# Kernel tuning notes

Measured on AMD Instinct MI355X. Metric: run time of the kernel, lower is better.

Reference implementation:

```python
import jax, jax.numpy as jnp
import numpy as np

N_X = 65536
N_IND = 1024
N_DESC = 64
INIT_LS = 10.0  # initial_lengthscale; params store -log(ls)


def setup_inputs() -> dict:
    key = jax.random.key(0)
    k1, k2, k3, k4 = jax.random.split(key, 4)
    x = jax.random.normal(k1, (N_X, N_DESC), dtype=jnp.float32)
    inducing_x = jax.random.normal(k2, (N_IND, N_DESC), dtype=jnp.float32)
    alpha = jax.random.normal(k3, (N_IND,), dtype=jnp.float32)
    # ARD lengthscales param, initialized near -log(initial_lengthscale) with jitter
    lengthscales = (-np.log(INIT_LS)
                    + 0.1 * jax.random.normal(k4, (N_DESC,), dtype=jnp.float32))
    return {"x": x, "inducing_x": inducing_x, "alpha": alpha,
            "lengthscales": lengthscales.astype(jnp.float32)}


def reference(x, inducing_x, alpha, lengthscales):
    # Squared distance weighted by per-descriptor lengthscale:
    #   d[i, j] = sum_k (x[j,k] - z[i,k])^2 / exp(ls[k])
    # Expanded as ||xw||^2 + ||zw||^2 - 2 zw @ xw^T to avoid the
    # (n_ind, n_x, n_desc) broadcast intermediate (same math).
    inv_sqrt_ls = jax.lax.rsqrt(jnp.exp(lengthscales))  # (n_desc,)
    xw = x * inv_sqrt_ls                                # (n_x, n_desc)
    zw = inducing_x * inv_sqrt_ls                       # (n_ind, n_desc)
    x_sq = jnp.sum(xw * xw, axis=-1)                    # (n_x,)
    z_sq = jnp.sum(zw * zw, axis=-1)                    # (n_ind,)
    cross = jnp.einsum('id,jd->ij', zw, xw)             # (n_ind, n_x)
    d = z_sq[:, None] + x_sq[None, :] - 2.0 * cross     # (n_ind, n_x)
    esd = jnp.exp(-d)                                   # RBF kernel matrix
    return (alpha @ esd)[:, None]                       # (n_x, 1)
```

## Files before the change

kernel.cpp:

```cpp
#include <hip/hip_runtime.h>
#include <hip/hip_bf16.h>

#define N_X    65536
#define N_IND  1024
#define N_DESC 64
#define TILES  (N_IND / 16)
#define L2E    1.4426950408889634f
#define L2E2   2.8853900817779268f
#define SKIP_THR (-60.0f)

typedef __attribute__((ext_vector_type(8))) short  short8;
typedef __attribute__((ext_vector_type(4))) float  f32x4;
typedef __attribute__((ext_vector_type(2))) float  f32x2;

static __device__ __forceinline__ ushort f2bf(float f) {
    union { float f; unsigned u; } a; a.f = f;
    unsigned r = a.u + 0x7FFF + ((a.u >> 16) & 1);
    return (ushort)(r >> 16);
}
static __device__ __forceinline__ float bf2f(ushort h) {
    union { unsigned u; float f; } a; a.u = (unsigned)h << 16;
    return a.f;
}

__global__ __launch_bounds__(1024) void igpr_fused(
        const float* __restrict__ x, const float* __restrict__ z,
        const float* __restrict__ alpha, const float* __restrict__ ls,
        float* __restrict__ out) {
    struct SM {
        uint4 zt[N_IND * 8];
        float z2[N_IND];
        float al[N_IND];
        float z2m[TILES];
    };
    __shared__ SM sm;

    const int tid  = threadIdx.x;
    const int lane = tid & 63;
    const int wave = tid >> 6;
    const int p = lane & 15;
    const int g = lane >> 4;
    const int j = blockIdx.x * 256 + wave * 16 + p;

    const float* xr = x + (size_t)j * N_DESC;
    float4 xv0 = *reinterpret_cast<const float4*>(xr + g * 8);
    float4 xv1 = *reinterpret_cast<const float4*>(xr + g * 8 + 4);
    float4 xv2 = *reinterpret_cast<const float4*>(xr + 32 + g * 8);
    float4 xv3 = *reinterpret_cast<const float4*>(xr + 32 + g * 8 + 4);
    float  alv = alpha[tid];

    const int gr = tid & 7;
    const int row_base = tid >> 3;
    float wz[8];
#pragma unroll
    for (int e = 0; e < 8; ++e) wz[e] = __expf(-0.5f * ls[gr * 8 + e]);

    char* zbw = reinterpret_cast<char*>(sm.zt);

#define ZLD(rb, A, B)                                                          \
    {                                                                          \
        const float* zp_ = z + (size_t)((rb) * 128 + row_base) * 64 + gr * 8;  \
        A = *reinterpret_cast<const float4*>(zp_);                             \
        B = *reinterpret_cast<const float4*>(zp_ + 4);                         \
    }
#define ZCVT(rb, A, B)                                                         \
    {                                                                          \
        float vv_[8] = {A.x, A.y, A.z, A.w, B.x, B.y, B.z, B.w};               \
        ushort hb_[8]; float sq_ = 0.f;                                        \
        _Pragma("unroll")                                                      \
        for (int e = 0; e < 8; ++e) {                                          \
            ushort h_ = f2bf(vv_[e] * wz[e]);                                  \
            hb_[e] = h_;                                                       \
            float vr_ = bf2f(h_);                                              \
            sq_ = fmaf(vr_, vr_, sq_);                                         \
        }                                                                      \
        uint4 u_ = make_uint4(                                                 \
            (unsigned)hb_[0] | ((unsigned)hb_[1] << 16),                       \
            (unsigned)hb_[2] | ((unsigned)hb_[3] << 16),                       \
            (unsigned)hb_[4] | ((unsigned)hb_[5] << 16),                       \
            (unsigned)hb_[6] | ((unsigned)hb_[7] << 16));                      \
        int row_ = (rb) * 128 + row_base;                                      \
        int sw_  = row_ * 128 + ((gr * 16) ^ ((row_ & 7) << 4));               \
        *reinterpret_cast<uint4*>(zbw + sw_) = u_;                             \
        sq_ += __shfl_xor(sq_, 1);                                             \
        sq_ += __shfl_xor(sq_, 2);                                             \
        sq_ += __shfl_xor(sq_, 4);                                             \
        if (gr == 0) sm.z2[row_] = sq_ * L2E;                                  \
    }

    float4 cA, cB, nA, nB;
    ZLD(0, cA, cB)
    ZLD(1, nA, nB)
    ZCVT(0, cA, cB)  ZLD(2, cA, cB)
    ZCVT(1, nA, nB)  ZLD(3, nA, nB)
    ZCVT(2, cA, cB)  ZLD(4, cA, cB)
    ZCVT(3, nA, nB)  ZLD(5, nA, nB)
    ZCVT(4, cA, cB)  ZLD(6, cA, cB)
    ZCVT(5, nA, nB)  ZLD(7, nA, nB)
    ZCVT(6, cA, cB)
    ZCVT(7, nA, nB)
#undef ZLD
#undef ZCVT

    sm.al[tid] = alv;

    short8 b0, b1;
    float xs2;
    {
        float wx[16];
#pragma unroll
        for (int h = 0; h < 2; ++h)
#pragma unroll
            for (int e = 0; e < 8; ++e)
                wx[h * 8 + e] = __expf(-0.5f * ls[h * 32 + g * 8 + e]);
        float vv[16] = {xv0.x, xv0.y, xv0.z, xv0.w, xv1.x, xv1.y, xv1.z, xv1.w,
                        xv2.x, xv2.y, xv2.z, xv2.w, xv3.x, xv3.y, xv3.z, xv3.w};
        float sq = 0.f;
        short8 bb[2];
#pragma unroll
        for (int h = 0; h < 2; ++h)
#pragma unroll
            for (int e = 0; e < 8; ++e) {
                ushort hh = f2bf(vv[h * 8 + e] * wx[h * 8 + e]);
                bb[h][e] = (short)hh;
                float xv = bf2f(hh);
                sq = fmaf(xv, xv, sq);
            }
        b0 = bb[0]; b1 = bb[1];
        sq += __shfl_xor(sq, 16);
        sq += __shfl_xor(sq, 32);
        xs2 = sq * L2E;
    }

    __syncthreads();

    if (tid < TILES) {
        float mn = sm.z2[tid * 16];
#pragma unroll
        for (int i = 1; i < 16; ++i) mn = fminf(mn, sm.z2[tid * 16 + i]);
        sm.z2m[tid] = mn;
    }

    __syncthreads();

    const char* zb = reinterpret_cast<const char*>(sm.zt);
    const int rb0 = p * 128 + ((16 * g)      ^ ((p & 7) << 4));
    const int rb1 = p * 128 + ((64 + 16 * g) ^ ((p & 7) << 4));

    f32x2 accJ = {0.f, 0.f};
    const f32x2 xs2p = {xs2, xs2};
    const float thr_base = SKIP_THR + xs2;

#pragma unroll 4
    for (int it = 0; it < TILES; ++it) {
        short8 a0 = *reinterpret_cast<const short8*>(zb + it * 2048 + rb0);
        short8 a1 = *reinterpret_cast<const short8*>(zb + it * 2048 + rb1);
        float zm = sm.z2m[it];

        f32x4 t = {0.f, 0.f, 0.f, 0.f};
        t = __builtin_amdgcn_mfma_f32_16x16x32_bf16(a0, b0, t, 0, 0, 0);
        t = __builtin_amdgcn_mfma_f32_16x16x32_bf16(a1, b1, t, 0, 0, 0);

        float maxdot = fmaxf(fmaxf(t[0], t[1]), fmaxf(t[2], t[3]));
        float bound  = fmaf(maxdot, L2E2, -zm);

        if (!__all(bound < thr_base)) {
            float4 z2 = *reinterpret_cast<const float4*>(&sm.z2[it * 16 + g * 4]);
            float4 a4 = *reinterpret_cast<const float4*>(&sm.al[it * 16 + g * 4]);
            f32x2 z2p0 = {z2.x, z2.y}, z2p1 = {z2.z, z2.w};
            f32x2 d0 = {t[0], t[1]}, d1 = {t[2], t[3]};
            f32x2 arg0 = d0 * L2E2 - (z2p0 + xs2p);
            f32x2 arg1 = d1 * L2E2 - (z2p1 + xs2p);
            f32x2 pv0 = {__builtin_amdgcn_exp2f(arg0.x),
                         __builtin_amdgcn_exp2f(arg0.y)};
            f32x2 pv1 = {__builtin_amdgcn_exp2f(arg1.x),
                         __builtin_amdgcn_exp2f(arg1.y)};
            f32x2 a4p0 = {a4.x, a4.y}, a4p1 = {a4.z, a4.w};
            accJ = accJ + a4p0 * pv0;
            accJ = accJ + a4p1 * pv1;
        }
    }

    float r = accJ.x + accJ.y;
    r += __shfl_xor(r, 16);
    r += __shfl_xor(r, 32);
    if (g == 0) out[j] = r;
}

extern "C" void kernel_launch(void* const* d_in, const int* in_sizes, int n_in,
                              void* d_out, int out_size, void* d_ws, size_t ws_size,
                              hipStream_t stream) {
    const float* x     = (const float*)d_in[0];
    const float* z     = (const float*)d_in[1];
    const float* alpha = (const float*)d_in[2];
    const float* ls    = (const float*)d_in[3];
    float* out = (float*)d_out;

    igpr_fused<<<dim3(N_X / 256), dim3(1024), 0, stream>>>(x, z, alpha, ls, out);
}
```

Before: 20.25 us.

## Split inducing points across blocks and process two x tiles per wave

Each block now stages only half of the inducing points in shared memory and handles 32 x rows per wave instead of 16, so each A-fragment read from LDS feeds two MFMA pairs. Partial sums from the two inducing-point chunks are combined with atomicAdd, which requires a separate zeroing kernel launch beforehand. The aim is to halve per-block z conversion and LDS footprint and raise operand reuse. The costs are an extra launch, atomic traffic, and a looser skip test that takes the minimum x norm of both tiles.

```diff
diff --git a/kernel.cpp b/kernel.cpp
--- a/kernel.cpp
+++ b/kernel.cpp
@@ -4,7 +4,9 @@
 #define N_X    65536
 #define N_IND  1024
 #define N_DESC 64
-#define TILES  (N_IND / 16)
+#define NCHUNK 2
+#define CROWS  (N_IND / NCHUNK)
+#define TILES  (CROWS / 16)
 #define L2E    1.4426950408889634f
 #define L2E2   2.8853900817779268f
 #define SKIP_THR (-60.0f)
@@ -21,6 +23,10 @@
 static __device__ __forceinline__ float bf2f(ushort h) {
     union { unsigned u; float f; } a; a.u = (unsigned)h << 16;
     return a.f;
+}
+
+__global__ __launch_bounds__(1024) void igpr_zero(float* __restrict__ out) {
+    out[blockIdx.x * 1024 + threadIdx.x] = 0.f;
 }
 
 __global__ __launch_bounds__(1024) void igpr_fused(
@@ -28,9 +34,9 @@
         const float* __restrict__ alpha, const float* __restrict__ ls,
         float* __restrict__ out) {
     struct SM {
-        uint4 zt[N_IND * 8];
-        float z2[N_IND];
-        float al[N_IND];
+        uint4 zt[CROWS * 8];
+        float z2[CROWS];
+        float al[CROWS];
         float z2m[TILES];
     };
     __shared__ SM sm;
@@ -40,14 +46,19 @@
     const int wave = tid >> 6;
     const int p = lane & 15;
     const int g = lane >> 4;
-    const int j = blockIdx.x * 256 + wave * 16 + p;
-
-    const float* xr = x + (size_t)j * N_DESC;
-    float4 xv0 = *reinterpret_cast<const float4*>(xr + g * 8);
-    float4 xv1 = *reinterpret_cast<const float4*>(xr + g * 8 + 4);
-    float4 xv2 = *reinterpret_cast<const float4*>(xr + 32 + g * 8);
-    float4 xv3 = *reinterpret_cast<const float4*>(xr + 32 + g * 8 + 4);
-    float  alv = alpha[tid];
+    const int c  = blockIdx.y;
+    const int j0 = blockIdx.x * 512 + wave * 32;
+
+    const float* xr0 = x + (size_t)(j0 + p) * N_DESC;
+    const float* xr1 = x + (size_t)(j0 + 16 + p) * N_DESC;
+    float4 xa0 = *reinterpret_cast<const float4*>(xr0 + g * 8);
+    float4 xa1 = *reinterpret_cast<const float4*>(xr0 + g * 8 + 4);
+    float4 xa2 = *reinterpret_cast<const float4*>(xr0 + 32 + g * 8);
+    float4 xa3 = *reinterpret_cast<const float4*>(xr0 + 32 + g * 8 + 4);
+    float4 xb0 = *reinterpret_cast<const float4*>(xr1 + g * 8);
+    float4 xb1 = *reinterpret_cast<const float4*>(xr1 + g * 8 + 4);
+    float4 xb2 = *reinterpret_cast<const float4*>(xr1 + 32 + g * 8);
+    float4 xb3 = *reinterpret_cast<const float4*>(xr1 + 32 + g * 8 + 4);
 
     const int gr = tid & 7;
     const int row_base = tid >> 3;
@@ -56,10 +67,11 @@
     for (int e = 0; e < 8; ++e) wz[e] = __expf(-0.5f * ls[gr * 8 + e]);
 
     char* zbw = reinterpret_cast<char*>(sm.zt);
+    const float* zc = z + (size_t)c * CROWS * N_DESC;
 
 #define ZLD(rb, A, B)                                                          \
     {                                                                          \
-        const float* zp_ = z + (size_t)((rb) * 128 + row_base) * 64 + gr * 8;  \
+        const float* zp_ = zc + (size_t)((rb) * 128 + row_base) * 64 + gr * 8; \
         A = *reinterpret_cast<const float4*>(zp_);                             \
         B = *reinterpret_cast<const float4*>(zp_ + 4);                         \
     }
@@ -88,24 +100,22 @@
         if (gr == 0) sm.z2[row_] = sq_ * L2E;                                  \
     }
 
-    float4 cA, cB, nA, nB;
-    ZLD(0, cA, cB)
-    ZLD(1, nA, nB)
-    ZCVT(0, cA, cB)  ZLD(2, cA, cB)
-    ZCVT(1, nA, nB)  ZLD(3, nA, nB)
-    ZCVT(2, cA, cB)  ZLD(4, cA, cB)
-    ZCVT(3, nA, nB)  ZLD(5, nA, nB)
-    ZCVT(4, cA, cB)  ZLD(6, cA, cB)
-    ZCVT(5, nA, nB)  ZLD(7, nA, nB)
-    ZCVT(6, cA, cB)
-    ZCVT(7, nA, nB)
+    {
+        float4 cA, cB, nA, nB;
+        ZLD(0, cA, cB)
+        ZLD(1, nA, nB)
+        ZCVT(0, cA, cB)  ZLD(2, cA, cB)
+        ZCVT(1, nA, nB)  ZLD(3, nA, nB)
+        ZCVT(2, cA, cB)
+        ZCVT(3, nA, nB)
+    }
 #undef ZLD
 #undef ZCVT
 
-    sm.al[tid] = alv;
-
-    short8 b0, b1;
-    float xs2;
+    if (tid < CROWS) sm.al[tid] = alpha[c * CROWS + tid];
+
+    short8 b[2][2];
+    float xs2v[2];
     {
         float wx[16];
 #pragma unroll
@@ -113,23 +123,30 @@
 #pragma unroll
             for (int e = 0; e < 8; ++e)
                 wx[h * 8 + e] = __expf(-0.5f * ls[h * 32 + g * 8 + e]);
-        float vv[16] = {xv0.x, xv0.y, xv0.z, xv0.w, xv1.x, xv1.y, xv1.z, xv1.w,
-                        xv2.x, xv2.y, xv2.z, xv2.w, xv3.x, xv3.y, xv3.z, xv3.w};
-        float sq = 0.f;
-        short8 bb[2];
-#pragma unroll
-        for (int h = 0; h < 2; ++h)
-#pragma unroll
-            for (int e = 0; e < 8; ++e) {
-                ushort hh = f2bf(vv[h * 8 + e] * wx[h * 8 + e]);
-                bb[h][e] = (short)hh;
-                float xv = bf2f(hh);
-                sq = fmaf(xv, xv, sq);
-            }
-        b0 = bb[0]; b1 = bb[1];
-        sq += __shfl_xor(sq, 16);
-        sq += __shfl_xor(sq, 32);
-        xs2 = sq * L2E;
+
+        float va[16] = {xa0.x, xa0.y, xa0.z, xa0.w, xa1.x, xa1.y, xa1.z, xa1.w,
+                        xa2.x, xa2.y, xa2.z, xa2.w, xa3.x, xa3.y, xa3.z, xa3.w};
+        float vb[16] = {xb0.x, xb0.y, xb0.z, xb0.w, xb1.x, xb1.y, xb1.z, xb1.w,
+                        xb2.x, xb2.y, xb2.z, xb2.w, xb3.x, xb3.y, xb3.z, xb3.w};
+#pragma unroll
+        for (int s = 0; s < 2; ++s) {
+            const float* vv = (s == 0) ? va : vb;
+            float sq = 0.f;
+            short8 bb[2];
+#pragma unroll
+            for (int h = 0; h < 2; ++h)
+#pragma unroll
+                for (int e = 0; e < 8; ++e) {
+                    ushort hh = f2bf(vv[h * 8 + e] * wx[h * 8 + e]);
+                    bb[h][e] = (short)hh;
+                    float xv = bf2f(hh);
+                    sq = fmaf(xv, xv, sq);
+                }
+            b[s][0] = bb[0]; b[s][1] = bb[1];
+            sq += __shfl_xor(sq, 16);
+            sq += __shfl_xor(sq, 32);
+            xs2v[s] = sq * L2E;
+        }
     }
 
     __syncthreads();
@@ -147,9 +164,8 @@
     const int rb0 = p * 128 + ((16 * g)      ^ ((p & 7) << 4));
     const int rb1 = p * 128 + ((64 + 16 * g) ^ ((p & 7) << 4));
 
-    f32x2 accJ = {0.f, 0.f};
-    const f32x2 xs2p = {xs2, xs2};
-    const float thr_base = SKIP_THR + xs2;
+    f32x2 accJ[2] = {{0.f, 0.f}, {0.f, 0.f}};
+    const float thr_base = SKIP_THR + fminf(xs2v[0], xs2v[1]);
 
 #pragma unroll 4
     for (int it = 0; it < TILES; ++it) {
@@ -157,34 +173,46 @@
         short8 a1 = *reinterpret_cast<const short8*>(zb + it * 2048 + rb1);
         float zm = sm.z2m[it];
 
-        f32x4 t = {0.f, 0.f, 0.f, 0.f};
-        t = __builtin_amdgcn_mfma_f32_16x16x32_bf16(a0, b0, t, 0, 0, 0);
-        t = __builtin_amdgcn_mfma_f32_16x16x32_bf16(a1, b1, t, 0, 0, 0);
-
-        float maxdot = fmaxf(fmaxf(t[0], t[1]), fmaxf(t[2], t[3]));
-        float bound  = fmaf(maxdot, L2E2, -zm);
+        f32x4 t0 = {0.f, 0.f, 0.f, 0.f};
+        t0 = __builtin_amdgcn_mfma_f32_16x16x32_bf16(a0, b[0][0], t0, 0, 0, 0);
+        t0 = __builtin_amdgcn_mfma_f32_16x16x32_bf16(a1, b[0][1], t0, 0, 0, 0);
+        f32x4 t1 = {0.f, 0.f, 0.f, 0.f};
+        t1 = __builtin_amdgcn_mfma_f32_16x16x32_bf16(a0, b[1][0], t1, 0, 0, 0);
+        t1 = __builtin_amdgcn_mfma_f32_16x16x32_bf16(a1, b[1][1], t1, 0, 0, 0);
+
+        float m0 = fmaxf(fmaxf(t0[0], t0[1]), fmaxf(t0[2], t0[3]));
+        float m1 = fmaxf(fmaxf(t1[0], t1[1]), fmaxf(t1[2], t1[3]));
+        float bound = fmaf(fmaxf(m0, m1), L2E2, -zm);
 
         if (!__all(bound < thr_base)) {
             float4 z2 = *reinterpret_cast<const float4*>(&sm.z2[it * 16 + g * 4]);
             float4 a4 = *reinterpret_cast<const float4*>(&sm.al[it * 16 + g * 4]);
             f32x2 z2p0 = {z2.x, z2.y}, z2p1 = {z2.z, z2.w};
-            f32x2 d0 = {t[0], t[1]}, d1 = {t[2], t[3]};
-            f32x2 arg0 = d0 * L2E2 - (z2p0 + xs2p);
-            f32x2 arg1 = d1 * L2E2 - (z2p1 + xs2p);
-            f32x2 pv0 = {__builtin_amdgcn_exp2f(arg0.x),
-                         __builtin_amdgcn_exp2f(arg0.y)};
-            f32x2 pv1 = {__builtin_amdgcn_exp2f(arg1.x),
-                         __builtin_amdgcn_exp2f(arg1.y)};
             f32x2 a4p0 = {a4.x, a4.y}, a4p1 = {a4.z, a4.w};
-            accJ = accJ + a4p0 * pv0;
-            accJ = accJ + a4p1 * pv1;
+#pragma unroll
+            for (int s = 0; s < 2; ++s) {
+                f32x4 t = (s == 0) ? t0 : t1;
+                f32x2 xsp = {xs2v[s], xs2v[s]};
+                f32x2 d0 = {t[0], t[1]}, d1 = {t[2], t[3]};
+                f32x2 arg0 = d0 * L2E2 - (z2p0 + xsp);
+                f32x2 arg1 = d1 * L2E2 - (z2p1 + xsp);
+                f32x2 pv0 = {__builtin_amdgcn_exp2f(arg0.x),
+                             __builtin_amdgcn_exp2f(arg0.y)};
+                f32x2 pv1 = {__builtin_amdgcn_exp2f(arg1.x),
+                             __builtin_amdgcn_exp2f(arg1.y)};
+                accJ[s] = accJ[s] + a4p0 * pv0;
+                accJ[s] = accJ[s] + a4p1 * pv1;
+            }
         }
     }
 
-    float r = accJ.x + accJ.y;
-    r += __shfl_xor(r, 16);
-    r += __shfl_xor(r, 32);
-    if (g == 0) out[j] = r;
+#pragma unroll
+    for (int s = 0; s < 2; ++s) {
+        float r = accJ[s].x + accJ[s].y;
+        r += __shfl_xor(r, 16);
+        r += __shfl_xor(r, 32);
+        if (g == 0) atomicAdd(&out[j0 + s * 16 + p], r);
+    }
 }
 
 extern "C" void kernel_launch(void* const* d_in, const int* in_sizes, int n_in,
@@ -196,5 +224,7 @@
     const float* ls    = (const float*)d_in[3];
     float* out = (float*)d_out;
 
-    igpr_fused<<<dim3(N_X / 256), dim3(1024), 0, stream>>>(x, z, alpha, ls, out);
-}
+    igpr_zero<<<dim3(N_X / 1024), dim3(1024), 0, stream>>>(out);
+    igpr_fused<<<dim3(N_X / 512, NCHUNK), dim3(1024), 0, stream>>>(
+        x, z, alpha, ls, out);
+}
```

Result: slower. 24.50 us (+21.0%).
